# Kernel tuning notes

Measured on AMD Instinct MI355X. Metric: run time of the kernel, lower is better.

The kernel has to match this reference:

```python
import jax, jax.numpy as jnp
import numpy as np

N_NODES = 100000
N_EDGES = 1600000
D_FEAT = 256
UNITS = 128
N_SUP = 2


def setup_inputs() -> dict:
    key = jax.random.key(0)
    ks = jax.random.split(key, 8)
    x = jax.random.normal(ks[0], (N_NODES, D_FEAT), dtype=jnp.float32)
    edge_vals = jax.random.uniform(ks[1], (N_SUP, N_EDGES), dtype=jnp.float32)
    W = jax.random.normal(ks[2], (N_SUP, D_FEAT, UNITS), dtype=jnp.float32) * 0.06  # ~glorot scale
    b = jnp.zeros((N_SUP, UNITS), dtype=jnp.float32)
    W_gate = jax.random.normal(ks[3], (N_SUP, D_FEAT, 1), dtype=jnp.float32) * 0.1
    b_gate = jnp.zeros((N_SUP, 1), dtype=jnp.float32)
    edge_rows = jax.random.randint(ks[4], (N_SUP, N_EDGES), 0, N_NODES, dtype=jnp.int32)
    edge_cols = jax.random.randint(ks[5], (N_SUP, N_EDGES), 0, N_NODES, dtype=jnp.int32)
    return {"x": x, "edge_vals": edge_vals, "W": W, "b": b,
            "W_gate": W_gate, "b_gate": b_gate,
            "edge_rows": edge_rows, "edge_cols": edge_cols}


def _spmm(rows, cols, vals, dense):
    # A @ dense where A is COO sparse [N, N]; dense is [N, U]
    msgs = vals[:, None] * dense[cols]  # [E, U]
    return jax.ops.segment_sum(msgs, rows, num_segments=N_NODES)


def reference(x, edge_vals, W, b, W_gate, b_gate, edge_rows, edge_cols):
    out = jnp.zeros((N_NODES, UNITS), dtype=x.dtype)
    for i in range(N_SUP):  # small fixed number of structurally distinct supports
        pre_sup = x @ W[i] + b[i]                           # [N, UNITS]
        g = jax.nn.sigmoid(x @ W_gate[i] + b_gate[i])       # [N, 1]
        out = out + _spmm(edge_rows[i], edge_cols[i], edge_vals[i], g * pre_sup)
    return jax.nn.relu(out)
```

## Files before the change

### kernel.cpp

```cpp
#include <hip/hip_runtime.h>
#include <hip/hip_bf16.h>

#define N_NODES 100000
#define N_EDGES 1600000
#define D_FEAT  256
#define UNITS   128
#define SLAB    48
#define NBKT    98
#define BKT_CAP 18432
#define NTILES  (N_NODES / 16)
#define NPAIR   ((NTILES + 7) / 8)
#define GEMM_BLKS (98 * 16)
#define SPLIT_BLKS 391
#define B_SHORTS (8 * 9 * 64 * 8)

typedef __attribute__((ext_vector_type(8))) short bf16x8;
typedef __attribute__((ext_vector_type(4))) float f32x4;
typedef __attribute__((ext_vector_type(2))) float f32x2;

__global__ __launch_bounds__(256) void pack_w_kernel(
    const float* __restrict__ W, const float* __restrict__ Wg,
    __hip_bfloat16* __restrict__ Bp) {
  const int idx = blockIdx.x * 256 + threadIdx.x;
  if (idx >= 2 * 8 * 9 * 64 * 8) return;
  const int j    = idx & 7;
  const int lane = (idx >> 3) & 63;
  const int cf   = (idx >> 9) % 9;
  const int ks   = (idx >> 9) / 9 % 8;
  const int s    = idx / (8 * 9 * 64 * 8);
  const int k    = ks * 32 + (lane >> 4) * 8 + j;
  float v;
  if (cf < 8) {
    const int col = cf * 16 + (lane & 15);
    v = W[((size_t)s * D_FEAT + k) * UNITS + col];
  } else {
    v = ((lane & 15) == 0) ? Wg[(size_t)s * D_FEAT + k] : 0.f;
  }
  Bp[idx] = __float2bfloat16(v);
}

__device__ __forceinline__ void gemm_body(
    const float* __restrict__ x, const __hip_bfloat16* __restrict__ Bp,
    const float* __restrict__ b, const float* __restrict__ bg,
    __hip_bfloat16* __restrict__ h, short* __restrict__ Blds, int pairBase) {
  const int tid  = threadIdx.x;
  const int lane = tid & 63;
  const int wave = tid >> 6;
  const int l15  = lane & 15;
  const int l4   = lane >> 4;
  const int tb   = pairBase * 8 + wave;
  const int rowbase = tb * 16;

  const int r0 = min(rowbase + l15, N_NODES - 1);
  const float4* __restrict__ a0p =
      (const float4*)(x + (size_t)r0 * D_FEAT) + l4 * 2;

  float4 xa[16];
#pragma unroll
  for (int ks = 0; ks < 8; ++ks) {
    xa[2 * ks]     = a0p[ks * 8];
    xa[2 * ks + 1] = a0p[ks * 8 + 1];
  }

  const float4* __restrict__ bp4 = (const float4*)Bp;
  float4*       __restrict__ ld4 = (float4*)Blds;
#pragma unroll
  for (int i = 0; i < 9; ++i)
    ld4[i * 512 + tid] = bp4[i * 512 + tid];
  __syncthreads();

  f32x4 acc[9];
#pragma unroll
  for (int cf = 0; cf < 9; ++cf) acc[cf] = (f32x4){0.f, 0.f, 0.f, 0.f};

#pragma unroll
  for (int ks = 0; ks < 8; ++ks) {
    const float4 lo = xa[2 * ks], hi = xa[2 * ks + 1];
    union { bf16x8 v; __hip_bfloat16 e[8]; } fa;
    fa.e[0] = __float2bfloat16(lo.x); fa.e[1] = __float2bfloat16(lo.y);
    fa.e[2] = __float2bfloat16(lo.z); fa.e[3] = __float2bfloat16(lo.w);
    fa.e[4] = __float2bfloat16(hi.x); fa.e[5] = __float2bfloat16(hi.y);
    fa.e[6] = __float2bfloat16(hi.z); fa.e[7] = __float2bfloat16(hi.w);
#pragma unroll
    for (int cf = 0; cf < 9; ++cf) {
      const bf16x8 fb = *(const bf16x8*)(Blds + ((ks * 9 + cf) * 64 + lane) * 8);
      acc[cf] = __builtin_amdgcn_mfma_f32_16x16x32_bf16(fa.v, fb, acc[cf], 0, 0, 0);
    }
  }

  const float bgv = bg[0];
  float bv[8];
#pragma unroll
  for (int cf = 0; cf < 8; ++cf) bv[cf] = b[cf * 16 + l15];

#pragma unroll
  for (int r = 0; r < 4; ++r) {
    const float gp = __shfl(acc[8][r], lane & 48);
    const float g  = 1.f / (1.f + __expf(-(gp + bgv)));
    const int row  = rowbase + l4 * 4 + r;
    if (row < N_NODES) {
#pragma unroll
      for (int cf = 0; cf < 8; ++cf) {
        const float val = g * (acc[cf][r] + bv[cf]);
        h[(size_t)row * UNITS + cf * 16 + l15] = __float2bfloat16(val);
      }
    }
  }
}

__device__ __forceinline__ void split_body(
    const int* __restrict__ rows, const int* __restrict__ cols,
    const float* __restrict__ vals, int* __restrict__ cursor,
    int2* __restrict__ grouped, int* __restrict__ shm, int chunk) {
  int* hist = shm;
  int* base = shm + NBKT;
  const int t  = threadIdx.x;
  const int e0 = chunk * 4096;

  for (int i = t; i < NBKT; i += 512) hist[i] = 0;
  __syncthreads();

  int rloc[8];
#pragma unroll
  for (int i = 0; i < 8; ++i) {
    const int e = e0 + i * 512 + t;
    if (e < N_EDGES) {
      rloc[i] = __builtin_nontemporal_load(rows + e);
      atomicAdd(&hist[rloc[i] >> 10], 1);
    }
  }
  __syncthreads();

  for (int i = t; i < NBKT; i += 512) {
    const int c = hist[i];
    base[i] = c ? atomicAdd(&cursor[i], c) : 0;
    hist[i] = 0;
  }
  __syncthreads();

#pragma unroll
  for (int i = 0; i < 8; ++i) {
    const int e = e0 + i * 512 + t;
    if (e < N_EDGES) {
      const int r   = rloc[i];
      const int bkt = r >> 10;
      const int pos = base[bkt] + atomicAdd(&hist[bkt], 1);
      if (pos < BKT_CAP) {
        const int   c = __builtin_nontemporal_load(cols + e);
        const float v = __builtin_nontemporal_load(vals + e);
        grouped[(size_t)bkt * BKT_CAP + pos] =
            make_int2((r & 1023) | (c << 10), __float2int_rn(v * 32767.f));
      }
    }
  }
}

__global__ __launch_bounds__(512, 4) void mega_kernel(
    const float* __restrict__ x, const __hip_bfloat16* __restrict__ Bp,
    const float* __restrict__ b, const float* __restrict__ bg,
    __hip_bfloat16* __restrict__ h0, __hip_bfloat16* __restrict__ h1,
    const int* __restrict__ er, const int* __restrict__ ec,
    const float* __restrict__ ev,
    int* __restrict__ cursor0, int* __restrict__ cursor1,
    int2* __restrict__ grouped0, int2* __restrict__ grouped1) {
  __shared__ short Blds[B_SHORTS];
  const int j = blockIdx.x;
  if (j < GEMM_BLKS) {
    const int r = j & 15;
    const int s = r >> 3;
    const int pairBase = (j >> 4) * 8 + (r & 7);
    if (pairBase >= NPAIR) return;
    gemm_body(x, Bp + (size_t)s * B_SHORTS, b + s * UNITS, bg + s,
              s ? h1 : h0, Blds, pairBase);
  } else {
    const int idx   = j - GEMM_BLKS;
    const int s     = idx >= SPLIT_BLKS;
    const int chunk = s ? idx - SPLIT_BLKS : idx;
    split_body(er + (size_t)s * N_EDGES, ec + (size_t)s * N_EDGES,
               ev + (size_t)s * N_EDGES,
               s ? cursor1 : cursor0, s ? grouped1 : grouped0,
               (int*)Blds, chunk);
  }
}

__global__ __launch_bounds__(512, 4) void gemm_mfma_kernel(
    const float* __restrict__ x, const __hip_bfloat16* __restrict__ Bp,
    const float* __restrict__ b, const float* __restrict__ bg,
    __hip_bfloat16* __restrict__ h) {
  __shared__ short Blds[B_SHORTS];
  gemm_body(x, Bp, b, bg, h, Blds, blockIdx.x);
}

__global__ __launch_bounds__(512) void split512_kernel(
    const int* __restrict__ rows, const int* __restrict__ cols,
    const float* __restrict__ vals, int* __restrict__ cursor,
    int2* __restrict__ grouped) {
  __shared__ int shm[2 * NBKT];
  split_body(rows, cols, vals, cursor, grouped, shm, blockIdx.x);
}

__global__ __launch_bounds__(1024) void bin_kernel(
    const int* __restrict__ cursor, const int2* __restrict__ grouped,
    int* __restrict__ deg, unsigned int* __restrict__ slab) {
  __shared__ int ldeg[1024];
  const int bkt = blockIdx.x;
  const int cnt = min(cursor[bkt], BKT_CAP);
  const int rowbase = bkt << 10;

  ldeg[threadIdx.x] = 0;
  __syncthreads();

  const int2* __restrict__ g = grouped + (size_t)bkt * BKT_CAP;
  for (int i = threadIdx.x; i < cnt; i += 1024) {
    const unsigned long long raw =
        __builtin_nontemporal_load((const unsigned long long*)(g + i));
    const int gx = (int)(raw & 0xffffffffu);
    const int gy = (int)(raw >> 32);
    const int rl  = gx & 1023;
    const int pos = atomicAdd(&ldeg[rl], 1);
    if (pos < SLAB)
      slab[(size_t)(rowbase + rl) * SLAB + pos] =
          (((unsigned int)gx >> 10) << 15) | (unsigned int)gy;
  }
  __syncthreads();

  const int row = rowbase + threadIdx.x;
  if (row < N_NODES) deg[row] = ldeg[threadIdx.x];
}

__device__ __forceinline__ void gath_acc(
    int d, int ent, const unsigned int* __restrict__ hb, int lane,
    float2& acc0, float2& acc1) {
  const float SC = 1.f / 32767.f;
  int e = 0;
  for (; e + 8 <= d; e += 8) {
    unsigned int u[8];
    float v[8];
#pragma unroll
    for (int i = 0; i < 8; ++i) {
      const unsigned int w = (unsigned int)__shfl(ent, e + i);
      v[i] = (float)(w & 0x7fffu) * SC;
      u[i] = hb[(size_t)(w >> 15) * 64 + lane];
    }
#pragma unroll
    for (int i = 0; i < 8; ++i) {
      float2& a = (i & 1) ? acc1 : acc0;
      a.x += v[i] * __uint_as_float(u[i] << 16);
      a.y += v[i] * __uint_as_float(u[i] & 0xffff0000u);
    }
  }
  if (e + 4 <= d) {
    unsigned int u[4];
    float v[4];
#pragma unroll
    for (int i = 0; i < 4; ++i) {
      const unsigned int w = (unsigned int)__shfl(ent, e + i);
      v[i] = (float)(w & 0x7fffu) * SC;
      u[i] = hb[(size_t)(w >> 15) * 64 + lane];
    }
#pragma unroll
    for (int i = 0; i < 4; ++i) {
      float2& a = (i & 1) ? acc1 : acc0;
      a.x += v[i] * __uint_as_float(u[i] << 16);
      a.y += v[i] * __uint_as_float(u[i] & 0xffff0000u);
    }
    e += 4;
  }
  for (; e < d; ++e) {
    const unsigned int w = (unsigned int)__shfl(ent, e);
    const float v = (float)(w & 0x7fffu) * SC;
    const unsigned int u = hb[(size_t)(w >> 15) * 64 + lane];
    acc0.x += v * __uint_as_float(u << 16);
    acc0.y += v * __uint_as_float(u & 0xffff0000u);
  }
}

__global__ __launch_bounds__(256) void gather_fused(
    const int* __restrict__ deg0, const unsigned int* __restrict__ slab0,
    const unsigned int* __restrict__ h0,
    const int* __restrict__ deg1, const unsigned int* __restrict__ slab1,
    const unsigned int* __restrict__ h1,
    float* __restrict__ out) {
  const int wave = threadIdx.x >> 6;
  const int lane = threadIdx.x & 63;
  const int row  = blockIdx.x * 4 + wave;
  const int d0   = min(__builtin_nontemporal_load(deg0 + row), SLAB);
  const int d1   = min(__builtin_nontemporal_load(deg1 + row), SLAB);

  int ent0 = 0, ent1 = 0;
  if (lane < d0) ent0 = (int)__builtin_nontemporal_load(slab0 + (size_t)row * SLAB + lane);
  if (lane < d1) ent1 = (int)__builtin_nontemporal_load(slab1 + (size_t)row * SLAB + lane);

  float2 acc0 = make_float2(0.f, 0.f);
  float2 acc1 = make_float2(0.f, 0.f);
  gath_acc(d0, ent0, h0, lane, acc0, acc1);
  gath_acc(d1, ent1, h1, lane, acc0, acc1);

  f32x2 o;
  o.x = fmaxf(acc0.x + acc1.x, 0.f);
  o.y = fmaxf(acc0.y + acc1.y, 0.f);
  __builtin_nontemporal_store(o, (f32x2*)out + (size_t)row * 64 + lane);
}

template <int LAST>
__global__ __launch_bounds__(256) void gather_one(
    const int* __restrict__ deg, const unsigned int* __restrict__ slab,
    const unsigned int* __restrict__ hbits, float* __restrict__ out) {
  const int wave = threadIdx.x >> 6;
  const int lane = threadIdx.x & 63;
  const int row  = blockIdx.x * 4 + wave;
  const int d    = min(deg[row], SLAB);

  int ent = 0;
  if (lane < d) ent = (int)__builtin_nontemporal_load(slab + (size_t)row * SLAB + lane);

  float2 acc0 = make_float2(0.f, 0.f);
  float2 acc1 = make_float2(0.f, 0.f);
  gath_acc(d, ent, hbits, lane, acc0, acc1);

  float2 acc = make_float2(acc0.x + acc1.x, acc0.y + acc1.y);
  float2* __restrict__ o2 = (float2*)out;
  const size_t oi = (size_t)row * 64 + lane;
  if (LAST) {
    const float2 prev = o2[oi];
    acc.x = fmaxf(prev.x + acc.x, 0.f);
    acc.y = fmaxf(prev.y + acc.y, 0.f);
  }
  o2[oi] = acc;
}

extern "C" void kernel_launch(void* const* d_in, const int* in_sizes, int n_in,
                              void* d_out, int out_size, void* d_ws, size_t ws_size,
                              hipStream_t stream) {
  const float* x         = (const float*)d_in[0];
  const float* edge_vals = (const float*)d_in[1];
  const float* W         = (const float*)d_in[2];
  const float* b         = (const float*)d_in[3];
  const float* Wg        = (const float*)d_in[4];
  const float* bg        = (const float*)d_in[5];
  const int*   er        = (const int*)d_in[6];
  const int*   ec        = (const int*)d_in[7];
  float* out = (float*)d_out;
  char* ws = (char*)d_ws;

  const size_t NEED = 105146624;

  if (ws_size >= NEED) {
    __hip_bfloat16* h0       = (__hip_bfloat16*)ws;
    __hip_bfloat16* h1       = (__hip_bfloat16*)(ws + 25600000);
    int*            deg0     = (int*)(ws + 51200000);
    int*            deg1     = (int*)(ws + 51600000);
    int*            cursor0  = (int*)(ws + 52000000);
    int*            cursor1  = (int*)(ws + 52000512);
    unsigned int*   slab0    = (unsigned int*)(ws + 52001024);
    unsigned int*   slab1    = (unsigned int*)(ws + 71201024);
    int2*           grouped0 = (int2*)(ws + 71201024);
    int2*           grouped1 = (int2*)(ws + 90401024);
    __hip_bfloat16* Bp       = (__hip_bfloat16*)(ws + 104851712);

    pack_w_kernel<<<(2 * 8 * 9 * 64 * 8 + 255) / 256, 256, 0, stream>>>(W, Wg, Bp);
    hipMemsetAsync(cursor0, 0, 1024, stream);

    mega_kernel<<<GEMM_BLKS + 2 * SPLIT_BLKS, 512, 0, stream>>>(
        x, Bp, b, bg, h0, h1, er, ec, edge_vals,
        cursor0, cursor1, grouped0, grouped1);

    bin_kernel<<<NBKT, 1024, 0, stream>>>(cursor0, grouped0, deg0, slab0);
    bin_kernel<<<NBKT, 1024, 0, stream>>>(cursor1, grouped1, deg1, slab1);

    gather_fused<<<N_NODES / 4, 256, 0, stream>>>(
        deg0, slab0, (const unsigned int*)h0,
        deg1, slab1, (const unsigned int*)h1, out);
  } else {
    __hip_bfloat16* h       = (__hip_bfloat16*)ws;
    int*            deg     = (int*)(ws + 25600000);
    int*            cursor  = (int*)(ws + 26000000);
    unsigned int*   slab    = (unsigned int*)(ws + 26000512);
    int2*           grouped = (int2*)(ws + 45200512);
    __hip_bfloat16* Bp      = (__hip_bfloat16*)(ws + 59651200);

    pack_w_kernel<<<(2 * 8 * 9 * 64 * 8 + 255) / 256, 256, 0, stream>>>(W, Wg, Bp);

    for (int s = 0; s < 2; ++s) {
      hipMemsetAsync(cursor, 0, 512, stream);
      gemm_mfma_kernel<<<NPAIR, 512, 0, stream>>>(
          x, Bp + (size_t)s * B_SHORTS, b + (size_t)s * UNITS, bg + s, h);
      split512_kernel<<<SPLIT_BLKS, 512, 0, stream>>>(
          er + (size_t)s * N_EDGES, ec + (size_t)s * N_EDGES,
          edge_vals + (size_t)s * N_EDGES, cursor, grouped);
      bin_kernel<<<NBKT, 1024, 0, stream>>>(cursor, grouped, deg, slab);
      if (s == 0) {
        gather_one<0><<<N_NODES / 4, 256, 0, stream>>>(deg, slab, (const unsigned int*)h, out);
      } else {
        gather_one<1><<<N_NODES / 4, 256, 0, stream>>>(deg, slab, (const unsigned int*)h, out);
      }
    }
  }
}
```

Before: 241.2 us.

## Pad slab rows to multiples of 8 and interleave both supports' gathers

The binning step now pads each row's slab entries with zero entries up to a multiple of 8, capped at SLAB, and stores the padded degree. That lets the gather kernels drop their 4-wide and scalar remainder loops and run only 8-wide blocks. The fused gather interleaves the 8-wide blocks of both supports, so loads from both feature tables can be in flight together before accumulating. A paired bin kernel that handles both supports in one launch is also added. The cost is extra padded entries to write and gather: they point at node 0 with zero weight, which wastes load bandwidth and gives slightly uneven control flow when the two supports' degrees differ.

```diff
diff --git a/kernel.cpp b/kernel.cpp
--- a/kernel.cpp
+++ b/kernel.cpp
@@ -199,19 +199,19 @@
   split_body(rows, cols, vals, cursor, grouped, shm, blockIdx.x);
 }
 
-__global__ __launch_bounds__(1024) void bin_kernel(
+__device__ __forceinline__ void bin_body(
     const int* __restrict__ cursor, const int2* __restrict__ grouped,
-    int* __restrict__ deg, unsigned int* __restrict__ slab) {
-  __shared__ int ldeg[1024];
-  const int bkt = blockIdx.x;
+    int* __restrict__ deg, unsigned int* __restrict__ slab,
+    int* __restrict__ ldeg, int bkt) {
+  const int t   = threadIdx.x;
   const int cnt = min(cursor[bkt], BKT_CAP);
   const int rowbase = bkt << 10;
 
-  ldeg[threadIdx.x] = 0;
+  ldeg[t] = 0;
   __syncthreads();
 
   const int2* __restrict__ g = grouped + (size_t)bkt * BKT_CAP;
-  for (int i = threadIdx.x; i < cnt; i += 1024) {
+  for (int i = t; i < cnt; i += 1024) {
     const unsigned long long raw =
         __builtin_nontemporal_load((const unsigned long long*)(g + i));
     const int gx = (int)(raw & 0xffffffffu);
@@ -224,55 +224,33 @@
   }
   __syncthreads();
 
-  const int row = rowbase + threadIdx.x;
-  if (row < N_NODES) deg[row] = ldeg[threadIdx.x];
-}
-
-__device__ __forceinline__ void gath_acc(
-    int d, int ent, const unsigned int* __restrict__ hb, int lane,
-    float2& acc0, float2& acc1) {
-  const float SC = 1.f / 32767.f;
-  int e = 0;
-  for (; e + 8 <= d; e += 8) {
-    unsigned int u[8];
-    float v[8];
-#pragma unroll
-    for (int i = 0; i < 8; ++i) {
-      const unsigned int w = (unsigned int)__shfl(ent, e + i);
-      v[i] = (float)(w & 0x7fffu) * SC;
-      u[i] = hb[(size_t)(w >> 15) * 64 + lane];
-    }
-#pragma unroll
-    for (int i = 0; i < 8; ++i) {
-      float2& a = (i & 1) ? acc1 : acc0;
-      a.x += v[i] * __uint_as_float(u[i] << 16);
-      a.y += v[i] * __uint_as_float(u[i] & 0xffff0000u);
-    }
-  }
-  if (e + 4 <= d) {
-    unsigned int u[4];
-    float v[4];
-#pragma unroll
-    for (int i = 0; i < 4; ++i) {
-      const unsigned int w = (unsigned int)__shfl(ent, e + i);
-      v[i] = (float)(w & 0x7fffu) * SC;
-      u[i] = hb[(size_t)(w >> 15) * 64 + lane];
-    }
-#pragma unroll
-    for (int i = 0; i < 4; ++i) {
-      float2& a = (i & 1) ? acc1 : acc0;
-      a.x += v[i] * __uint_as_float(u[i] << 16);
-      a.y += v[i] * __uint_as_float(u[i] & 0xffff0000u);
-    }
-    e += 4;
-  }
-  for (; e < d; ++e) {
-    const unsigned int w = (unsigned int)__shfl(ent, e);
-    const float v = (float)(w & 0x7fffu) * SC;
-    const unsigned int u = hb[(size_t)(w >> 15) * 64 + lane];
-    acc0.x += v * __uint_as_float(u << 16);
-    acc0.y += v * __uint_as_float(u & 0xffff0000u);
-  }
+  const int row = rowbase + t;
+  if (row < N_NODES) {
+    const int d    = min(ldeg[t], SLAB);
+    const int dpad = min((d + 7) & ~7, SLAB);
+    for (int p = d; p < dpad; ++p)
+      slab[(size_t)row * SLAB + p] = 0u;
+    deg[row] = dpad;
+  }
+}
+
+__global__ __launch_bounds__(1024) void bin_pair_kernel(
+    const int* __restrict__ cursor0, const int2* __restrict__ grouped0,
+    int* __restrict__ deg0, unsigned int* __restrict__ slab0,
+    const int* __restrict__ cursor1, const int2* __restrict__ grouped1,
+    int* __restrict__ deg1, unsigned int* __restrict__ slab1) {
+  __shared__ int ldeg[1024];
+  const int s   = blockIdx.x & 1;
+  const int bkt = blockIdx.x >> 1;
+  if (s == 0) bin_body(cursor0, grouped0, deg0, slab0, ldeg, bkt);
+  else        bin_body(cursor1, grouped1, deg1, slab1, ldeg, bkt);
+}
+
+__global__ __launch_bounds__(1024) void bin_kernel(
+    const int* __restrict__ cursor, const int2* __restrict__ grouped,
+    int* __restrict__ deg, unsigned int* __restrict__ slab) {
+  __shared__ int ldeg[1024];
+  bin_body(cursor, grouped, deg, slab, ldeg, blockIdx.x);
 }
 
 __global__ __launch_bounds__(256) void gather_fused(
@@ -284,21 +262,64 @@
   const int wave = threadIdx.x >> 6;
   const int lane = threadIdx.x & 63;
   const int row  = blockIdx.x * 4 + wave;
-  const int d0   = min(__builtin_nontemporal_load(deg0 + row), SLAB);
-  const int d1   = min(__builtin_nontemporal_load(deg1 + row), SLAB);
+  const int d0   = deg0[row];
+  const int d1   = deg1[row];
 
   int ent0 = 0, ent1 = 0;
   if (lane < d0) ent0 = (int)__builtin_nontemporal_load(slab0 + (size_t)row * SLAB + lane);
   if (lane < d1) ent1 = (int)__builtin_nontemporal_load(slab1 + (size_t)row * SLAB + lane);
 
-  float2 acc0 = make_float2(0.f, 0.f);
-  float2 acc1 = make_float2(0.f, 0.f);
-  gath_acc(d0, ent0, h0, lane, acc0, acc1);
-  gath_acc(d1, ent1, h1, lane, acc0, acc1);
+  const float SC = 1.f / 32767.f;
+  float2 accA = make_float2(0.f, 0.f);
+  float2 accB = make_float2(0.f, 0.f);
+
+  const int nb0 = d0 >> 3;
+  const int nb1 = d1 >> 3;
+  const int nb  = max(nb0, nb1);
+
+  for (int bi = 0; bi < nb; ++bi) {
+    const int e = bi * 8;
+    unsigned int u0[8], u1[8];
+    float v0[8], v1[8];
+    const bool go0 = bi < nb0;
+    const bool go1 = bi < nb1;
+    if (go0) {
+#pragma unroll
+      for (int i = 0; i < 8; ++i) {
+        const unsigned int w = (unsigned int)__shfl(ent0, e + i);
+        v0[i] = (float)(w & 0x7fffu) * SC;
+        u0[i] = h0[(size_t)(w >> 15) * 64 + lane];
+      }
+    }
+    if (go1) {
+#pragma unroll
+      for (int i = 0; i < 8; ++i) {
+        const unsigned int w = (unsigned int)__shfl(ent1, e + i);
+        v1[i] = (float)(w & 0x7fffu) * SC;
+        u1[i] = h1[(size_t)(w >> 15) * 64 + lane];
+      }
+    }
+    if (go0) {
+#pragma unroll
+      for (int i = 0; i < 8; ++i) {
+        float2& a = (i & 1) ? accB : accA;
+        a.x += v0[i] * __uint_as_float(u0[i] << 16);
+        a.y += v0[i] * __uint_as_float(u0[i] & 0xffff0000u);
+      }
+    }
+    if (go1) {
+#pragma unroll
+      for (int i = 0; i < 8; ++i) {
+        float2& a = (i & 1) ? accB : accA;
+        a.x += v1[i] * __uint_as_float(u1[i] << 16);
+        a.y += v1[i] * __uint_as_float(u1[i] & 0xffff0000u);
+      }
+    }
+  }
 
   f32x2 o;
-  o.x = fmaxf(acc0.x + acc1.x, 0.f);
-  o.y = fmaxf(acc0.y + acc1.y, 0.f);
+  o.x = fmaxf(accA.x + accB.x, 0.f);
+  o.y = fmaxf(accA.y + accB.y, 0.f);
   __builtin_nontemporal_store(o, (f32x2*)out + (size_t)row * 64 + lane);
 }
 
@@ -309,16 +330,34 @@
   const int wave = threadIdx.x >> 6;
   const int lane = threadIdx.x & 63;
   const int row  = blockIdx.x * 4 + wave;
-  const int d    = min(deg[row], SLAB);
+  const int d    = deg[row];
 
   int ent = 0;
   if (lane < d) ent = (int)__builtin_nontemporal_load(slab + (size_t)row * SLAB + lane);
 
-  float2 acc0 = make_float2(0.f, 0.f);
-  float2 acc1 = make_float2(0.f, 0.f);
-  gath_acc(d, ent, hbits, lane, acc0, acc1);
-
-  float2 acc = make_float2(acc0.x + acc1.x, acc0.y + acc1.y);
+  const float SC = 1.f / 32767.f;
+  float2 accA = make_float2(0.f, 0.f);
+  float2 accB = make_float2(0.f, 0.f);
+  const int nb = d >> 3;
+  for (int bi = 0; bi < nb; ++bi) {
+    const int e = bi * 8;
+    unsigned int u[8];
+    float v[8];
+#pragma unroll
+    for (int i = 0; i < 8; ++i) {
+      const unsigned int w = (unsigned int)__shfl(ent, e + i);
+      v[i] = (float)(w & 0x7fffu) * SC;
+      u[i] = hbits[(size_t)(w >> 15) * 64 + lane];
+    }
+#pragma unroll
+    for (int i = 0; i < 8; ++i) {
+      float2& a = (i & 1) ? accB : accA;
+      a.x += v[i] * __uint_as_float(u[i] << 16);
+      a.y += v[i] * __uint_as_float(u[i] & 0xffff0000u);
+    }
+  }
+
+  float2 acc = make_float2(accA.x + accB.x, accA.y + accB.y);
   float2* __restrict__ o2 = (float2*)out;
   const size_t oi = (size_t)row * 64 + lane;
   if (LAST) {
```

Result: no change. 243.4 us (+0.9%).

## Merge both supports' binning into one launch and pad slab degrees to eight

Applied to the files above, without the earlier changes.

Adds a paired binning kernel that processes both supports' buckets in a single launch, using a larger workspace layout so grouped and slab buffers no longer alias. It also pads each row's slab entries with zeros up to a multiple of eight and stores the padded degree, so the gather can run only its unrolled-by-eight loop without a remainder tail. In exchange, gathers do extra zero-weight loads, and the path runs only when the workspace is large enough. The old per-support path is kept as a fallback.

```diff
diff --git a/kernel.cpp b/kernel.cpp
--- a/kernel.cpp
+++ b/kernel.cpp
@@ -199,19 +199,19 @@
   split_body(rows, cols, vals, cursor, grouped, shm, blockIdx.x);
 }
 
-__global__ __launch_bounds__(1024) void bin_kernel(
+__device__ __forceinline__ void bin_body(
     const int* __restrict__ cursor, const int2* __restrict__ grouped,
-    int* __restrict__ deg, unsigned int* __restrict__ slab) {
-  __shared__ int ldeg[1024];
-  const int bkt = blockIdx.x;
+    int* __restrict__ deg, unsigned int* __restrict__ slab,
+    int* __restrict__ ldeg, int bkt) {
+  const int t   = threadIdx.x;
   const int cnt = min(cursor[bkt], BKT_CAP);
   const int rowbase = bkt << 10;
 
-  ldeg[threadIdx.x] = 0;
+  ldeg[t] = 0;
   __syncthreads();
 
   const int2* __restrict__ g = grouped + (size_t)bkt * BKT_CAP;
-  for (int i = threadIdx.x; i < cnt; i += 1024) {
+  for (int i = t; i < cnt; i += 1024) {
     const unsigned long long raw =
         __builtin_nontemporal_load((const unsigned long long*)(g + i));
     const int gx = (int)(raw & 0xffffffffu);
@@ -224,8 +224,33 @@
   }
   __syncthreads();
 
-  const int row = rowbase + threadIdx.x;
-  if (row < N_NODES) deg[row] = ldeg[threadIdx.x];
+  const int row = rowbase + t;
+  if (row < N_NODES) {
+    const int d    = min(ldeg[t], SLAB);
+    const int dpad = min((d + 7) & ~7, SLAB);
+    for (int p = d; p < dpad; ++p)
+      slab[(size_t)row * SLAB + p] = 0u;
+    deg[row] = dpad;
+  }
+}
+
+__global__ __launch_bounds__(1024) void bin_pair_kernel(
+    const int* __restrict__ cursor0, const int2* __restrict__ grouped0,
+    int* __restrict__ deg0, unsigned int* __restrict__ slab0,
+    const int* __restrict__ cursor1, const int2* __restrict__ grouped1,
+    int* __restrict__ deg1, unsigned int* __restrict__ slab1) {
+  __shared__ int ldeg[1024];
+  const int s   = blockIdx.x & 1;
+  const int bkt = blockIdx.x >> 1;
+  if (s == 0) bin_body(cursor0, grouped0, deg0, slab0, ldeg, bkt);
+  else        bin_body(cursor1, grouped1, deg1, slab1, ldeg, bkt);
+}
+
+__global__ __launch_bounds__(1024) void bin_kernel(
+    const int* __restrict__ cursor, const int2* __restrict__ grouped,
+    int* __restrict__ deg, unsigned int* __restrict__ slab) {
+  __shared__ int ldeg[1024];
+  bin_body(cursor, grouped, deg, slab, ldeg, blockIdx.x);
 }
 
 __device__ __forceinline__ void gath_acc(
@@ -343,9 +368,36 @@
   float* out = (float*)d_out;
   char* ws = (char*)d_ws;
 
-  const size_t NEED = 105146624;
-
-  if (ws_size >= NEED) {
+  const size_t NEED2 = 119597312;
+  const size_t NEED  = 105146624;
+
+  if (ws_size >= NEED2) {
+    __hip_bfloat16* h0       = (__hip_bfloat16*)ws;
+    __hip_bfloat16* h1       = (__hip_bfloat16*)(ws + 25600000);
+    int*            deg0     = (int*)(ws + 51200000);
+    int*            deg1     = (int*)(ws + 51600000);
+    int*            cursor0  = (int*)(ws + 52000000);
+    int*            cursor1  = (int*)(ws + 52000512);
+    unsigned int*   slab0    = (unsigned int*)(ws + 52001024);
+    unsigned int*   slab1    = (unsigned int*)(ws + 71201024);
+    int2*           grouped0 = (int2*)(ws + 90401024);
+    int2*           grouped1 = (int2*)(ws + 104851712);
+    __hip_bfloat16* Bp       = (__hip_bfloat16*)(ws + 119302400);
+
+    pack_w_kernel<<<(2 * 8 * 9 * 64 * 8 + 255) / 256, 256, 0, stream>>>(W, Wg, Bp);
+    hipMemsetAsync(cursor0, 0, 1024, stream);
+
+    mega_kernel<<<GEMM_BLKS + 2 * SPLIT_BLKS, 512, 0, stream>>>(
+        x, Bp, b, bg, h0, h1, er, ec, edge_vals,
+        cursor0, cursor1, grouped0, grouped1);
+
+    bin_pair_kernel<<<2 * NBKT, 1024, 0, stream>>>(
+        cursor0, grouped0, deg0, slab0, cursor1, grouped1, deg1, slab1);
+
+    gather_fused<<<N_NODES / 4, 256, 0, stream>>>(
+        deg0, slab0, (const unsigned int*)h0,
+        deg1, slab1, (const unsigned int*)h1, out);
+  } else if (ws_size >= NEED) {
     __hip_bfloat16* h0       = (__hip_bfloat16*)ws;
     __hip_bfloat16* h1       = (__hip_bfloat16*)(ws + 25600000);
     int*            deg0     = (int*)(ws + 51200000);
```

New measurement: 230.1 us. 4.6% less time.
